# Kernel optimization log

Measured on AMD Instinct MI355X. Metric: run time of the kernel, lower is better.

Reference implementation:

```python
import jax, jax.numpy as jnp
import numpy as np


def _rope(x, pos, theta):
    # x: [b, s, h, d], pos: [s] int. Standard interleaved RoPE on even/odd pairs.
    d = x.shape[-1]
    inv_freq = theta ** (-jnp.arange(0, d, 2, dtype=jnp.float32) / d)  # [d/2]
    ang = pos.astype(jnp.float32)[:, None] * inv_freq                  # [s, d/2]
    cos = jnp.cos(ang)[None, :, None, :]
    sin = jnp.sin(ang)[None, :, None, :]
    x1 = x[..., 0::2]
    x2 = x[..., 1::2]
    rot = jnp.stack([x1 * cos - x2 * sin, x1 * sin + x2 * cos], axis=-1)
    return rot.reshape(x.shape)


def setup_inputs() -> dict:
    key = jax.random.key(0)
    ks = jax.random.split(key, 5)
    b, s, d = 4, 2048, 1024
    scale = 1.0 / np.sqrt(d)
    return {
        "x": jax.random.normal(ks[0], (b, s, d), dtype=jnp.float32),
        "W_Q": jax.random.normal(ks[1], (d, d), dtype=jnp.float32) * scale,
        "W_K": jax.random.normal(ks[2], (d, d), dtype=jnp.float32) * scale,
        "W_V": jax.random.normal(ks[3], (d, d), dtype=jnp.float32) * scale,
        "W_O": jax.random.normal(ks[4], (d, d), dtype=jnp.float32) * scale,
        "token_positions": jnp.arange(s, dtype=jnp.int32),
    }


def reference(x, W_Q, W_K, W_V, W_O, token_positions):
    num_heads = 16
    theta = 10000.0
    b, s, d_model = x.shape
    d_k = d_model // num_heads

    Q = x @ W_Q.T  # [b, s, d_model]
    K = x @ W_K.T
    V = x @ W_V.T

    # split heads: last dim is [h0 | h1 | ...] so reshape to [b, s, h, d_k]
    Qh = Q.reshape(b, s, num_heads, d_k)
    Kh = K.reshape(b, s, num_heads, d_k)
    Vh = V.reshape(b, s, num_heads, d_k)

    Qh = _rope(Qh, token_positions, theta)
    Kh = _rope(Kh, token_positions, theta)

    scores = jnp.einsum("bqhd,bkhd->bhqk", Qh, Kh) / jnp.sqrt(
        jnp.asarray(d_k, dtype=x.dtype)
    )
    causal = jnp.tril(jnp.ones((s, s), dtype=bool))  # True = keep
    scores = jnp.where(causal[None, None, :, :], scores, jnp.asarray(-jnp.inf, x.dtype))
    probs = jax.nn.softmax(scores, axis=-1)

    out = jnp.einsum("bhqk,bkhd->bqhd", probs, Vh).reshape(b, s, d_model)
    return out @ W_O.T
```

## Files before the change

kernel.cpp:

```cpp
#include <hip/hip_runtime.h>
#include <hip/hip_bf16.h>
#include <type_traits>

typedef __attribute__((ext_vector_type(8))) short short8;
typedef __attribute__((ext_vector_type(4))) short s16x4;
typedef __attribute__((ext_vector_type(4))) float f32x4;
typedef unsigned short u16;
typedef unsigned int   u32;
typedef unsigned long long u64;


#if __has_builtin(__builtin_amdgcn_mfma_f32_16x16x16bf16_1k)
#define MFMA16(a, b, c) __builtin_amdgcn_mfma_f32_16x16x16bf16_1k(a, b, c, 0, 0, 0)
#define HAVE_MFMA16 1
#elif __has_builtin(__builtin_amdgcn_mfma_f32_16x16x16_bf16)
#define MFMA16(a, b, c) __builtin_amdgcn_mfma_f32_16x16x16_bf16(a, b, c, 0, 0, 0)
#define HAVE_MFMA16 1
#else
#define HAVE_MFMA16 0
#endif

static __device__ __forceinline__ u16 f2b(float f) {
  u32 u = __builtin_bit_cast(u32, f);
  u = (u + 0x7fffu + ((u >> 16) & 1u)) >> 16;
  return (u16)u;
}
static __device__ __forceinline__ float b2f(u16 h) {
  return __builtin_bit_cast(float, ((u32)h) << 16);
}
static __device__ __forceinline__ u32 pkbf(float a, float b) {
  union { __hip_bfloat162 t; u32 u; } c;
  c.t = __float22bfloat162_rn(make_float2(a, b));
  return c.u;
}

typedef __attribute__((address_space(1))) const unsigned int gas_u32;
typedef __attribute__((address_space(3))) unsigned int las_u32;
static __device__ __forceinline__ void glds16(const u16* g, u16* l) {
  __builtin_amdgcn_global_load_lds((gas_u32*)g, (las_u32*)l, 16, 0, 0);
}

__global__ __launch_bounds__(256) void cvt_all(
    const float* __restrict__ x, const float* __restrict__ wq,
    const float* __restrict__ wk, const float* __restrict__ wv,
    const float* __restrict__ wo, u16* __restrict__ xb, u16* __restrict__ wqb,
    u16* __restrict__ wkb, u16* __restrict__ wvb, u16* __restrict__ wob) {
  int u = blockIdx.x * 256 + threadIdx.x;
  if (u >= 3145728) return;
  const float* src; u16* dst; int off;
  if (u < 2097152) { src = x; dst = xb; off = u; }
  else {
    int t = u - 2097152;
    int w = t >> 18;
    off = t & 0x3FFFF;
    src = (w == 0) ? wq : (w == 1) ? wk : (w == 2) ? wv : wo;
    dst = (w == 0) ? wqb : (w == 1) ? wkb : (w == 2) ? wvb : wob;
  }
  int i = off * 4;
  float4 v = *(const float4*)(src + i);
  union { u16 us[4]; u64 ull; } o;
  o.us[0] = f2b(v.x); o.us[1] = f2b(v.y); o.us[2] = f2b(v.z); o.us[3] = f2b(v.w);
  *(u64*)(dst + i) = o.ull;
}

template <typename OT>
static __device__ __forceinline__ void gemm_body(const u16* __restrict__ A,
                                                 const u16* __restrict__ B,
                                                 OT* __restrict__ C,
                                                 int m0, int n0) {
  __shared__ u16 As[4096];
  __shared__ u16 Bs[4096];

  const int tid  = threadIdx.x;
  const int lane = tid & 63;
  const int wv   = tid >> 6;
  const int quad = lane >> 4;
  const int cc   = lane & 15;
  const int wr   = wv >> 1;
  const int wc   = wv & 1;

  f32x4 acc[4][4];
#pragma unroll
  for (int i = 0; i < 4; i++)
#pragma unroll
    for (int j = 0; j < 4; j++) acc[i][j] = (f32x4){0.f, 0.f, 0.f, 0.f};

  const int p0 = wv * 128 + lane;
  const int p1 = p0 + 64;
  const int r0 = p0 >> 2, g0 = (p0 & 3) ^ (r0 & 3);
  const int r1 = p1 >> 2, g1 = (p1 & 3) ^ (r1 & 3);
  const u16* gA0 = A + (size_t)(m0 + r0) * 1024 + g0 * 8;
  const u16* gA1 = A + (size_t)(m0 + r1) * 1024 + g1 * 8;
  const u16* gB0 = B + (size_t)(n0 + r0) * 1024 + g0 * 8;
  const u16* gB1 = B + (size_t)(n0 + r1) * 1024 + g1 * 8;
  u16* lA = As + wv * 1024;
  u16* lB = Bs + wv * 1024;

  for (int k0 = 0; k0 < 1024; k0 += 32) {
    __syncthreads();
    glds16(gA0 + k0, lA);
    glds16(gA1 + k0, lA + 512);
    glds16(gB0 + k0, lB);
    glds16(gB1 + k0, lB + 512);
    __syncthreads();

    short8 af[4], bf[4];
#pragma unroll
    for (int mt = 0; mt < 4; mt++) {
      int ra = wr * 64 + mt * 16 + cc;
      af[mt] = *(const short8*)&As[ra * 32 + ((quad ^ (ra & 3)) * 8)];
    }
#pragma unroll
    for (int nt = 0; nt < 4; nt++) {
      int rb = wc * 64 + nt * 16 + cc;
      bf[nt] = *(const short8*)&Bs[rb * 32 + ((quad ^ (rb & 3)) * 8)];
    }
#pragma unroll
    for (int mt = 0; mt < 4; mt++)
#pragma unroll
      for (int nt = 0; nt < 4; nt++)
        acc[mt][nt] = __builtin_amdgcn_mfma_f32_16x16x32_bf16(af[mt], bf[nt], acc[mt][nt], 0, 0, 0);
  }

#pragma unroll
  for (int mt = 0; mt < 4; mt++)
#pragma unroll
    for (int nt = 0; nt < 4; nt++)
#pragma unroll
      for (int r = 0; r < 4; r++) {
        int row = m0 + wr * 64 + mt * 16 + quad * 4 + r;
        int col = n0 + wc * 64 + nt * 16 + cc;
        if constexpr (std::is_same_v<OT, float>)
          C[(size_t)row * 1024 + col] = acc[mt][nt][r];
        else
          C[(size_t)row * 1024 + col] = f2b(acc[mt][nt][r]);
      }
}

__global__ __launch_bounds__(256) void gemm_qkv(const u16* __restrict__ A,
                                                const u16* __restrict__ Bq,
                                                const u16* __restrict__ Bk,
                                                const u16* __restrict__ Bv,
                                                u16* __restrict__ Q,
                                                u16* __restrict__ K,
                                                u16* __restrict__ V) {
  int sel = blockIdx.x >> 3;
  const u16* B = (sel == 0) ? Bq : (sel == 1) ? Bk : Bv;
  u16* C = (sel == 0) ? Q : (sel == 1) ? K : V;
  gemm_body<u16>(A, B, C, blockIdx.y * 128, (blockIdx.x & 7) * 128);
}

__global__ __launch_bounds__(256) void gemm_out(const u16* __restrict__ A,
                                                const u16* __restrict__ B,
                                                float* __restrict__ C) {
  gemm_body<float>(A, B, C, blockIdx.y * 128, blockIdx.x * 128);
}

__global__ __launch_bounds__(256) void rope_kernel(u16* __restrict__ Q,
                                                   u16* __restrict__ K,
                                                   const int* __restrict__ pos) {
  u16* T = blockIdx.y ? K : Q;
  const float sc = blockIdx.y ? 1.0f : 0.125f;
  int idx = blockIdx.x * 256 + threadIdx.x;
  int row = idx >> 9;
  int p   = idx & 511;
  int i   = p & 31;
  int col = (p >> 5) * 64 + 2 * i;
  int s   = row & 2047;
  float ps  = (float)pos[s];
  float inv = exp2f(-(float)i * 0.41524101186092033f);
  float ang = ps * inv;
  float sn, cs;
  sincosf(ang, &sn, &cs);
  u32 v = *(u32*)(T + (size_t)row * 1024 + col);
  float x1 = b2f((u16)(v & 0xffffu));
  float x2 = b2f((u16)(v >> 16));
  float y1 = (x1 * cs - x2 * sn) * sc;
  float y2 = (x1 * sn + x2 * cs) * sc;
  *(u32*)(T + (size_t)row * 1024 + col) = (u32)f2b(y1) | ((u32)f2b(y2) << 16);
}

__global__ __launch_bounds__(256) void transpose_v(const u16* __restrict__ V,
                                                   u16* __restrict__ Vt) {
  __shared__ u16 t[64][65];
  int s0 = blockIdx.x * 64;
  int bh = blockIdx.y;
  int b = bh >> 4, h = bh & 15;
  int tid = threadIdx.x;
  int r = tid >> 2, ch = (tid & 3) * 16;
  const u16* src = V + (size_t)(b * 2048 + s0 + r) * 1024 + h * 64 + ch;
  union { uint4 v[2]; u16 us[16]; } tmp;
  tmp.v[0] = *(const uint4*)src;
  tmp.v[1] = *(const uint4*)(src + 8);
#pragma unroll
  for (int j = 0; j < 16; j++) t[r][ch + j] = tmp.us[j];
  __syncthreads();
  union { uint4 v[2]; u16 us[16]; } o;
#pragma unroll
  for (int j = 0; j < 16; j++) o.us[j] = t[ch + j][r];
  u16* dst = Vt + (size_t)(bh * 64 + r) * 2048 + s0 + ch;
  *(uint4*)dst = o.v[0];
  *(uint4*)(dst + 8) = o.v[1];
}

__global__ __launch_bounds__(256) void attn_kernel(const u16* __restrict__ Q,
                                                   const u16* __restrict__ K,
                                                   const u16* __restrict__ Vt,
                                                   u16* __restrict__ O) {
  __shared__ u16 Ks[8192];
  __shared__ u16 Vs[8192];
#if !HAVE_MFMA16
  __shared__ u16 Ps[4 * 16 * 136];
#endif

  const int bh = blockIdx.x;
  const int qt = 15 - blockIdx.y;
  const int b = bh >> 4, h = bh & 15;
  const int tid  = threadIdx.x;
  const int lane = tid & 63;
  const int wv   = tid >> 6;
  const int quad = lane >> 4;
  const int cc   = lane & 15;
  const int q0   = qt * 128;

  short8 qf[2][2];
#pragma unroll
  for (int mt = 0; mt < 2; mt++) {
    const u16* qp = Q + (size_t)(b * 2048 + q0 + wv * 32 + mt * 16 + cc) * 1024 + h * 64;
    qf[mt][0] = *(const short8*)(qp + quad * 8);
    qf[mt][1] = *(const short8*)(qp + 32 + quad * 8);
  }

  f32x4 o_acc[2][4];
  float m_i[2] = {-3.0e38f, -3.0e38f}, l_i[2] = {0.f, 0.f};
#pragma unroll
  for (int mt = 0; mt < 2; mt++)
#pragma unroll
    for (int nt = 0; nt < 4; nt++) o_acc[mt][nt] = (f32x4){0.f, 0.f, 0.f, 0.f};

  const u16* Kp = K + ((size_t)(b * 2048) + wv * 32 + (lane >> 3)) * 1024 + h * 64 +
                  (((lane & 7) ^ (lane >> 3)) * 8);
  const u16* Vp[4];
#pragma unroll
  for (int j = 0; j < 4; j++) {
    int rl = wv * 16 + j * 4 + (lane >> 4);
    int g  = ((lane & 15) - rl) & 15;
    Vp[j] = Vt + ((size_t)(bh * 64) + rl) * 2048 + g * 8;
  }

  const int nkt = qt + 1;
  const int pk0 = (quad ^ (cc & 7)) * 8;

  for (int kt = 0; kt < nkt; ++kt) {
    __syncthreads();
#pragma unroll
    for (int j = 0; j < 4; j++) {
      glds16(Kp + (size_t)kt * 131072 + j * 8192, Ks + wv * 2048 + j * 512);
      glds16(Vp[j] + kt * 128, Vs + wv * 2048 + j * 512);
    }
    __syncthreads();

    const bool diag = (kt == qt);

#pragma unroll
    for (int mt = 0; mt < 2; ++mt) {
      f32x4 s[8];
#pragma unroll
      for (int nt = 0; nt < 8; ++nt) {
        const int rbase = (nt * 16 + cc) * 64;
        short8 bk0 = *(const short8*)&Ks[rbase + pk0];
        short8 bk1 = *(const short8*)&Ks[rbase + (pk0 ^ 32)];
        f32x4 z = (f32x4){0.f, 0.f, 0.f, 0.f};
        z = __builtin_amdgcn_mfma_f32_16x16x32_bf16(bk0, qf[mt][0], z, 0, 0, 0);
        s[nt] = __builtin_amdgcn_mfma_f32_16x16x32_bf16(bk1, qf[mt][1], z, 0, 0, 0);
      }

      if (diag) {
        const int qg = q0 + wv * 32 + mt * 16 + cc;
        const int kb = kt * 128 + quad * 4;
#pragma unroll
        for (int nt = 0; nt < 8; ++nt)
#pragma unroll
          for (int r = 0; r < 4; ++r)
            if (kb + nt * 16 + r > qg) s[nt][r] = -3.0e38f;
      }

      float mx = s[0][0];
#pragma unroll
      for (int nt = 0; nt < 8; ++nt)
#pragma unroll
        for (int r = 0; r < 4; ++r) mx = fmaxf(mx, s[nt][r]);
      mx = fmaxf(mx, __shfl_xor(mx, 16));
      mx = fmaxf(mx, __shfl_xor(mx, 32));
      const float mn = fmaxf(m_i[mt], mx);
      const float al = __expf(m_i[mt] - mn);
      m_i[mt] = mn;

      s16x4 pf[8];
      float ps = 0.f;
#pragma unroll
      for (int nt = 0; nt < 8; ++nt) {
        float e0 = __expf(s[nt][0] - mn);
        float e1 = __expf(s[nt][1] - mn);
        float e2 = __expf(s[nt][2] - mn);
        float e3 = __expf(s[nt][3] - mn);
        ps += (e0 + e1) + (e2 + e3);
        union { u32 w[2]; s16x4 v; } pu;
        pu.w[0] = pkbf(e0, e1);
        pu.w[1] = pkbf(e2, e3);
        pf[nt] = pu.v;
      }
      l_i[mt] = l_i[mt] * al + ps;

      f32x4 al4;
#pragma unroll
      for (int r = 0; r < 4; ++r) al4[r] = __shfl(al, quad * 4 + r);
#pragma unroll
      for (int nt = 0; nt < 4; ++nt) o_acc[mt][nt] *= al4;

#if HAVE_MFMA16
#pragma unroll
      for (int nt = 0; nt < 4; ++nt) {
        const int rv = (nt * 16 + cc) * 128;
#pragma unroll
        for (int kk = 0; kk < 8; ++kk) {
          const int pos = (kk * 2 + (quad >> 1) + cc) & 15;
          s16x4 bv = *(const s16x4*)&Vs[rv + pos * 8 + (quad & 1) * 4];
          o_acc[mt][nt] = MFMA16(pf[kk], bv, o_acc[mt][nt]);
        }
      }
#else
#pragma unroll
      for (int nt = 0; nt < 8; ++nt) {
        union { s16x4 v; u64 ull; } pu2; pu2.v = pf[nt];
        *(u64*)&Ps[(wv * 16 + cc) * 136 + nt * 16 + quad * 4] = pu2.ull;
      }
      short8 pa[4];
#pragma unroll
      for (int ks = 0; ks < 4; ++ks)
        pa[ks] = *(const short8*)&Ps[(wv * 16 + cc) * 136 + ks * 32 + quad * 8];
#pragma unroll
      for (int nt = 0; nt < 4; ++nt) {
        const int rv = (nt * 16 + cc) * 128;
#pragma unroll
        for (int ks = 0; ks < 4; ++ks) {
          const int pos = (ks * 4 + quad + cc) & 15;
          short8 bv = *(const short8*)&Vs[rv + pos * 8];
          o_acc[mt][nt] = __builtin_amdgcn_mfma_f32_16x16x32_bf16(pa[ks], bv, o_acc[mt][nt], 0, 0, 0);
        }
      }
#endif
    }
  }

#pragma unroll
  for (int mt = 0; mt < 2; ++mt) {
    float l = l_i[mt];
    l += __shfl_xor(l, 16);
    l += __shfl_xor(l, 32);
    const float linv = 1.0f / l;
    f32x4 li4;
#pragma unroll
    for (int r = 0; r < 4; ++r) li4[r] = __shfl(linv, quad * 4 + r);
    const int rowb = b * 2048 + q0 + wv * 32 + mt * 16 + quad * 4;
#pragma unroll
    for (int nt = 0; nt < 4; ++nt)
#pragma unroll
      for (int r = 0; r < 4; ++r)
        O[(size_t)(rowb + r) * 1024 + h * 64 + nt * 16 + cc] = f2b(o_acc[mt][nt][r] * li4[r]);
  }
}

extern "C" void kernel_launch(void* const* d_in, const int* in_sizes, int n_in,
                              void* d_out, int out_size, void* d_ws, size_t ws_size,
                              hipStream_t stream) {
  const float* x  = (const float*)d_in[0];
  const float* wq = (const float*)d_in[1];
  const float* wk = (const float*)d_in[2];
  const float* wv = (const float*)d_in[3];
  const float* wo = (const float*)d_in[4];
  const int* pos  = (const int*)d_in[5];
  float* out = (float*)d_out;

  char* ws = (char*)d_ws;
  u16* xb  = (u16*)(ws);
  u16* vt  = (u16*)(ws);
  u16* wqb = (u16*)(ws + (16ull << 20));
  u16* wkb = (u16*)(ws + (18ull << 20));
  u16* wvb = (u16*)(ws + (20ull << 20));
  u16* wob = (u16*)(ws + (22ull << 20));
  u16* Qb  = (u16*)(ws + (24ull << 20));
  u16* Kb  = (u16*)(ws + (40ull << 20));
  u16* Vb  = (u16*)(ws + (56ull << 20));
  u16* aO  = Vb;

  cvt_all<<<12288, 256, 0, stream>>>(x, wq, wk, wv, wo, xb, wqb, wkb, wvb, wob);
  gemm_qkv<<<dim3(24, 64), 256, 0, stream>>>(xb, wqb, wkb, wvb, Qb, Kb, Vb);
  rope_kernel<<<dim3(16384, 2), 256, 0, stream>>>(Qb, Kb, pos);
  transpose_v<<<dim3(32, 64), 256, 0, stream>>>(Vb, vt);
  attn_kernel<<<dim3(64, 16), 256, 0, stream>>>(Qb, Kb, vt, aO);
  gemm_out<<<dim3(8, 64), 256, 0, stream>>>(aO, wob, out);
}
```

Baseline: 299.0 us.

## Pair causal query tiles per block, double-buffer K/V, use exp2 softmax

Each attention block now handles two query tiles (qt and 15-qt), so every block runs exactly 17 key tiles and the grid halves, balancing the causal triangle. K/V tiles are double-buffered in shared memory so the next tile's global-to-LDS load overlaps compute, dropping one barrier per iteration. Softmax moves to exp2 by folding log2(e) into the Q scale. V transpose reorders keys so one 8-wide LDS read feeds two 16x16x16 MFMAs shared across both m-tiles. The cost is doubled LDS use, which may lower occupancy.

```diff
diff --git a/kernel.cpp b/kernel.cpp
--- a/kernel.cpp
+++ b/kernel.cpp
@@ -10,15 +10,17 @@
 typedef unsigned long long u64;
 
 
-#if __has_builtin(__builtin_amdgcn_mfma_f32_16x16x16bf16_1k)
-#define MFMA16(a, b, c) __builtin_amdgcn_mfma_f32_16x16x16bf16_1k(a, b, c, 0, 0, 0)
-#define HAVE_MFMA16 1
-#elif __has_builtin(__builtin_amdgcn_mfma_f32_16x16x16_bf16)
-#define MFMA16(a, b, c) __builtin_amdgcn_mfma_f32_16x16x16_bf16(a, b, c, 0, 0, 0)
-#define HAVE_MFMA16 1
+#if defined(__HIP_DEVICE_COMPILE__)
+  #if __has_builtin(__builtin_amdgcn_mfma_f32_16x16x16bf16_1k)
+    #define MFMA16(a, b, c) __builtin_amdgcn_mfma_f32_16x16x16bf16_1k(a, b, c, 0, 0, 0)
+  #else
+    #define MFMA16(a, b, c) __builtin_amdgcn_mfma_f32_16x16x16_bf16(a, b, c, 0, 0, 0)
+  #endif
 #else
-#define HAVE_MFMA16 0
+  #define MFMA16(a, b, c) (c)
 #endif
+
+#define EXP2F(x) exp2f(x)
 
 static __device__ __forceinline__ u16 f2b(float f) {
   u32 u = __builtin_bit_cast(u32, f);
@@ -160,7 +162,7 @@
                                                    u16* __restrict__ K,
                                                    const int* __restrict__ pos) {
   u16* T = blockIdx.y ? K : Q;
-  const float sc = blockIdx.y ? 1.0f : 0.125f;
+  const float sc = blockIdx.y ? 1.0f : 0.18033688011112042f;
   int idx = blockIdx.x * 256 + threadIdx.x;
   int row = idx >> 9;
   int p   = idx & 511;
@@ -197,7 +199,11 @@
   __syncthreads();
   union { uint4 v[2]; u16 us[16]; } o;
 #pragma unroll
-  for (int j = 0; j < 16; j++) o.us[j] = t[ch + j][r];
+  for (int j = 0; j < 16; j++) {
+    int p  = ch + j;
+    int kg = (p & ~31) + ((p >> 2) & 1) * 16 + (((p & 31) >> 3) * 4) + (p & 3);
+    o.us[j] = t[kg][r];
+  }
   u16* dst = Vt + (size_t)(bh * 64 + r) * 2048 + s0 + ch;
   *(uint4*)dst = o.v[0];
   *(uint4*)(dst + 8) = o.v[1];
@@ -207,28 +213,29 @@
                                                    const u16* __restrict__ K,
                                                    const u16* __restrict__ Vt,
                                                    u16* __restrict__ O) {
-  __shared__ u16 Ks[8192];
-  __shared__ u16 Vs[8192];
-#if !HAVE_MFMA16
-  __shared__ u16 Ps[4 * 16 * 136];
-#endif
+  __shared__ u16 Ks[2][8192];
+  __shared__ u16 Vs[2][8192];
 
   const int bh = blockIdx.x;
-  const int qt = 15 - blockIdx.y;
+  const int y  = blockIdx.y;
+  const int qtA = 15 - y, qtB = y;
+  const int nA = qtA + 1;
   const int b = bh >> 4, h = bh & 15;
   const int tid  = threadIdx.x;
   const int lane = tid & 63;
   const int wv   = tid >> 6;
   const int quad = lane >> 4;
   const int cc   = lane & 15;
-  const int q0   = qt * 128;
-
-  short8 qf[2][2];
+
+  short8 qcur[2][2], qfB[2][2];
 #pragma unroll
   for (int mt = 0; mt < 2; mt++) {
-    const u16* qp = Q + (size_t)(b * 2048 + q0 + wv * 32 + mt * 16 + cc) * 1024 + h * 64;
-    qf[mt][0] = *(const short8*)(qp + quad * 8);
-    qf[mt][1] = *(const short8*)(qp + 32 + quad * 8);
+    const u16* qa = Q + (size_t)(b * 2048 + qtA * 128 + wv * 32 + mt * 16 + cc) * 1024 + h * 64;
+    qcur[mt][0] = *(const short8*)(qa + quad * 8);
+    qcur[mt][1] = *(const short8*)(qa + 32 + quad * 8);
+    const u16* qb = Q + (size_t)(b * 2048 + qtB * 128 + wv * 32 + mt * 16 + cc) * 1024 + h * 64;
+    qfB[mt][0] = *(const short8*)(qb + quad * 8);
+    qfB[mt][1] = *(const short8*)(qb + 32 + quad * 8);
   }
 
   f32x4 o_acc[2][4];
@@ -244,131 +251,153 @@
 #pragma unroll
   for (int j = 0; j < 4; j++) {
     int rl = wv * 16 + j * 4 + (lane >> 4);
-    int g  = ((lane & 15) - rl) & 15;
-    Vp[j] = Vt + ((size_t)(bh * 64) + rl) * 2048 + g * 8;
-  }
-
-  const int nkt = qt + 1;
+    int cl = ((lane & 15) - rl) & 15;
+    Vp[j] = Vt + ((size_t)(bh * 64) + rl) * 2048 + cl * 8;
+  }
+
+  auto stage = [&](int kt, int pp) {
+    u16* kb = &Ks[pp][wv * 2048];
+    u16* vb = &Vs[pp][wv * 2048];
+#pragma unroll
+    for (int j = 0; j < 4; j++) {
+      glds16(Kp + (size_t)kt * 131072 + j * 8192, kb + j * 512);
+      glds16(Vp[j] + kt * 128, vb + j * 512);
+    }
+  };
+
+  auto store_O = [&](int q0) {
+#pragma unroll
+    for (int mt = 0; mt < 2; ++mt) {
+      float l = l_i[mt];
+      l += __shfl_xor(l, 16);
+      l += __shfl_xor(l, 32);
+      const float linv = 1.0f / l;
+      f32x4 li4;
+#pragma unroll
+      for (int r = 0; r < 4; ++r) li4[r] = __shfl(linv, quad * 4 + r);
+      const int rowb = b * 2048 + q0 + wv * 32 + mt * 16 + quad * 4;
+#pragma unroll
+      for (int nt = 0; nt < 4; ++nt)
+#pragma unroll
+        for (int r = 0; r < 4; ++r)
+          O[(size_t)(rowb + r) * 1024 + h * 64 + nt * 16 + cc] =
+              f2b(o_acc[mt][nt][r] * li4[r]);
+    }
+  };
+
   const int pk0 = (quad ^ (cc & 7)) * 8;
 
-  for (int kt = 0; kt < nkt; ++kt) {
+  stage(0, 0);
+  int p = 0;
+
+  for (int it = 0; it < 17; ++it) {
+    const bool inA = it < nA;
+    const int kt = inA ? it : it - nA;
+    const int qt = inA ? qtA : qtB;
+
     __syncthreads();
-#pragma unroll
-    for (int j = 0; j < 4; j++) {
-      glds16(Kp + (size_t)kt * 131072 + j * 8192, Ks + wv * 2048 + j * 512);
-      glds16(Vp[j] + kt * 128, Vs + wv * 2048 + j * 512);
-    }
-    __syncthreads();
-
-    const bool diag = (kt == qt);
-
+
+    if (it + 1 < 17) {
+      int kt2 = (it + 1 < nA) ? it + 1 : it + 1 - nA;
+      stage(kt2, p ^ 1);
+    }
+
+    f32x4 s[2][8];
+#pragma unroll
+    for (int nt = 0; nt < 8; ++nt) {
+      const int rbase = (nt * 16 + cc) * 64;
+      short8 bk0 = *(const short8*)&Ks[p][rbase + pk0];
+      short8 bk1 = *(const short8*)&Ks[p][rbase + (pk0 ^ 32)];
+#pragma unroll
+      for (int mt = 0; mt < 2; ++mt) {
+        f32x4 z = (f32x4){0.f, 0.f, 0.f, 0.f};
+        z = __builtin_amdgcn_mfma_f32_16x16x32_bf16(bk0, qcur[mt][0], z, 0, 0, 0);
+        s[mt][nt] = __builtin_amdgcn_mfma_f32_16x16x32_bf16(bk1, qcur[mt][1], z, 0, 0, 0);
+      }
+    }
+
+    if (kt == qt) {
+#pragma unroll
+      for (int mt = 0; mt < 2; ++mt) {
+        const int qloc = wv * 32 + mt * 16 + cc;
+        const int kb = quad * 4;
+#pragma unroll
+        for (int nt = 0; nt < 8; ++nt)
+#pragma unroll
+          for (int r = 0; r < 4; ++r)
+            if (kb + nt * 16 + r > qloc) s[mt][nt][r] = -3.0e38f;
+      }
+    }
+
+    s16x4 pf[2][8];
+    float al[2];
 #pragma unroll
     for (int mt = 0; mt < 2; ++mt) {
-      f32x4 s[8];
-#pragma unroll
-      for (int nt = 0; nt < 8; ++nt) {
-        const int rbase = (nt * 16 + cc) * 64;
-        short8 bk0 = *(const short8*)&Ks[rbase + pk0];
-        short8 bk1 = *(const short8*)&Ks[rbase + (pk0 ^ 32)];
-        f32x4 z = (f32x4){0.f, 0.f, 0.f, 0.f};
-        z = __builtin_amdgcn_mfma_f32_16x16x32_bf16(bk0, qf[mt][0], z, 0, 0, 0);
-        s[nt] = __builtin_amdgcn_mfma_f32_16x16x32_bf16(bk1, qf[mt][1], z, 0, 0, 0);
-      }
-
-      if (diag) {
-        const int qg = q0 + wv * 32 + mt * 16 + cc;
-        const int kb = kt * 128 + quad * 4;
-#pragma unroll
-        for (int nt = 0; nt < 8; ++nt)
-#pragma unroll
-          for (int r = 0; r < 4; ++r)
-            if (kb + nt * 16 + r > qg) s[nt][r] = -3.0e38f;
-      }
-
-      float mx = s[0][0];
+      float mx = s[mt][0][0];
 #pragma unroll
       for (int nt = 0; nt < 8; ++nt)
 #pragma unroll
-        for (int r = 0; r < 4; ++r) mx = fmaxf(mx, s[nt][r]);
+        for (int r = 0; r < 4; ++r) mx = fmaxf(mx, s[mt][nt][r]);
       mx = fmaxf(mx, __shfl_xor(mx, 16));
       mx = fmaxf(mx, __shfl_xor(mx, 32));
       const float mn = fmaxf(m_i[mt], mx);
-      const float al = __expf(m_i[mt] - mn);
+      al[mt] = EXP2F(m_i[mt] - mn);
       m_i[mt] = mn;
 
-      s16x4 pf[8];
       float ps = 0.f;
 #pragma unroll
       for (int nt = 0; nt < 8; ++nt) {
-        float e0 = __expf(s[nt][0] - mn);
-        float e1 = __expf(s[nt][1] - mn);
-        float e2 = __expf(s[nt][2] - mn);
-        float e3 = __expf(s[nt][3] - mn);
+        float e0 = EXP2F(s[mt][nt][0] - mn);
+        float e1 = EXP2F(s[mt][nt][1] - mn);
+        float e2 = EXP2F(s[mt][nt][2] - mn);
+        float e3 = EXP2F(s[mt][nt][3] - mn);
         ps += (e0 + e1) + (e2 + e3);
         union { u32 w[2]; s16x4 v; } pu;
         pu.w[0] = pkbf(e0, e1);
         pu.w[1] = pkbf(e2, e3);
-        pf[nt] = pu.v;
-      }
-      l_i[mt] = l_i[mt] * al + ps;
+        pf[mt][nt] = pu.v;
+      }
+      l_i[mt] = l_i[mt] * al[mt] + ps;
 
       f32x4 al4;
 #pragma unroll
-      for (int r = 0; r < 4; ++r) al4[r] = __shfl(al, quad * 4 + r);
+      for (int r = 0; r < 4; ++r) al4[r] = __shfl(al[mt], quad * 4 + r);
 #pragma unroll
       for (int nt = 0; nt < 4; ++nt) o_acc[mt][nt] *= al4;
-
-#if HAVE_MFMA16
-#pragma unroll
-      for (int nt = 0; nt < 4; ++nt) {
-        const int rv = (nt * 16 + cc) * 128;
-#pragma unroll
-        for (int kk = 0; kk < 8; ++kk) {
-          const int pos = (kk * 2 + (quad >> 1) + cc) & 15;
-          s16x4 bv = *(const s16x4*)&Vs[rv + pos * 8 + (quad & 1) * 4];
-          o_acc[mt][nt] = MFMA16(pf[kk], bv, o_acc[mt][nt]);
+    }
+
+#pragma unroll
+    for (int nt = 0; nt < 4; ++nt) {
+      const int rv = (nt * 16 + cc) * 128;
+#pragma unroll
+      for (int g = 0; g < 4; ++g) {
+        short8 bv = *(const short8*)&Vs[p][rv + (((g * 4 + quad) + cc) & 15) * 8];
+        s16x4 lo = __builtin_shufflevector(bv, bv, 0, 1, 2, 3);
+        s16x4 hi = __builtin_shufflevector(bv, bv, 4, 5, 6, 7);
+#pragma unroll
+        for (int mt = 0; mt < 2; ++mt) {
+          o_acc[mt][nt] = MFMA16(pf[mt][2 * g], lo, o_acc[mt][nt]);
+          o_acc[mt][nt] = MFMA16(pf[mt][2 * g + 1], hi, o_acc[mt][nt]);
         }
       }
-#else
-#pragma unroll
-      for (int nt = 0; nt < 8; ++nt) {
-        union { s16x4 v; u64 ull; } pu2; pu2.v = pf[nt];
-        *(u64*)&Ps[(wv * 16 + cc) * 136 + nt * 16 + quad * 4] = pu2.ull;
-      }
-      short8 pa[4];
-#pragma unroll
-      for (int ks = 0; ks < 4; ++ks)
-        pa[ks] = *(const short8*)&Ps[(wv * 16 + cc) * 136 + ks * 32 + quad * 8];
-#pragma unroll
-      for (int nt = 0; nt < 4; ++nt) {
-        const int rv = (nt * 16 + cc) * 128;
-#pragma unroll
-        for (int ks = 0; ks < 4; ++ks) {
-          const int pos = (ks * 4 + quad + cc) & 15;
-          short8 bv = *(const short8*)&Vs[rv + pos * 8];
-          o_acc[mt][nt] = __builtin_amdgcn_mfma_f32_16x16x32_bf16(pa[ks], bv, o_acc[mt][nt], 0, 0, 0);
-        }
-      }
-#endif
-    }
-  }
-
-#pragma unroll
-  for (int mt = 0; mt < 2; ++mt) {
-    float l = l_i[mt];
-    l += __shfl_xor(l, 16);
-    l += __shfl_xor(l, 32);
-    const float linv = 1.0f / l;
-    f32x4 li4;
-#pragma unroll
-    for (int r = 0; r < 4; ++r) li4[r] = __shfl(linv, quad * 4 + r);
-    const int rowb = b * 2048 + q0 + wv * 32 + mt * 16 + quad * 4;
-#pragma unroll
-    for (int nt = 0; nt < 4; ++nt)
-#pragma unroll
-      for (int r = 0; r < 4; ++r)
-        O[(size_t)(rowb + r) * 1024 + h * 64 + nt * 16 + cc] = f2b(o_acc[mt][nt][r] * li4[r]);
-  }
+    }
+
+    if (it == nA - 1) {
+      store_O(qtA * 128);
+      m_i[0] = m_i[1] = -3.0e38f;
+      l_i[0] = l_i[1] = 0.f;
+#pragma unroll
+      for (int mt = 0; mt < 2; mt++) {
+#pragma unroll
+        for (int nt = 0; nt < 4; nt++) o_acc[mt][nt] = (f32x4){0.f, 0.f, 0.f, 0.f};
+        qcur[mt][0] = qfB[mt][0];
+        qcur[mt][1] = qfB[mt][1];
+      }
+    }
+    p ^= 1;
+  }
+
+  store_O(qtB * 128);
 }
 
 extern "C" void kernel_launch(void* const* d_in, const int* in_sizes, int n_in,
@@ -398,6 +427,6 @@
   gemm_qkv<<<dim3(24, 64), 256, 0, stream>>>(xb, wqb, wkb, wvb, Qb, Kb, Vb);
   rope_kernel<<<dim3(16384, 2), 256, 0, stream>>>(Qb, Kb, pos);
   transpose_v<<<dim3(32, 64), 256, 0, stream>>>(Vb, vt);
-  attn_kernel<<<dim3(64, 16), 256, 0, stream>>>(Qb, Kb, vt, aO);
+  attn_kernel<<<dim3(64, 8), 256, 0, stream>>>(Qb, Kb, vt, aO);
   gemm_out<<<dim3(8, 64), 256, 0, stream>>>(aO, wob, out);
 }
```

After: 338.6 us. 13.2% more time.
